# Kernel tuning notes

Hardware: AMD Instinct MI355X
Metric: run time of the kernel (lower is better)

Reference implementation:

```python
import jax, jax.numpy as jnp
import numpy as np

B, T, C = 2, 2048, 1024
H = 16
D = C // H  # head_dim = 64
SCALE = D ** -0.5


def setup_inputs() -> dict:
    key = jax.random.key(0)
    ks = jax.random.split(key, 5)
    s = 0.02
    return {
        "x": jax.random.normal(ks[0], (B, T, C), dtype=jnp.float32),
        "w_qkv": jax.random.normal(ks[1], (C, 3 * C), dtype=jnp.float32) * s,
        "b_qkv": jnp.zeros((3 * C,), dtype=jnp.float32),
        "w_proj": jax.random.normal(ks[2], (C, C), dtype=jnp.float32) * s,
        "b_proj": jnp.zeros((C,), dtype=jnp.float32),
    }


def reference(x, w_qkv, b_qkv, w_proj, b_proj):
    Bx, Tx, Cx = x.shape
    qkv = x @ w_qkv + b_qkv                      # [B,T,3C]
    q, k, v = jnp.split(qkv, 3, axis=-1)
    # [B,T,C] -> [B,H,T,D]
    q = q.reshape(Bx, Tx, H, D).transpose(0, 2, 1, 3)
    k = k.reshape(Bx, Tx, H, D).transpose(0, 2, 1, 3)
    v = v.reshape(Bx, Tx, H, D).transpose(0, 2, 1, 3)
    attn = jnp.einsum('bhqd,bhkd->bhqk', q, k) * SCALE
    causal = jnp.tril(jnp.ones((Tx, Tx), dtype=bool))
    attn = jnp.where(causal[None, None], attn, -jnp.inf)
    attn = jax.nn.softmax(attn, axis=-1)
    out = jnp.einsum('bhqk,bhkd->bhqd', attn, v)  # [B,H,T,D]
    out = out.transpose(0, 2, 1, 3).reshape(Bx, Tx, Cx)
    return out @ w_proj + b_proj
```

## Files before the change

### kernel.cpp

```cpp
#include <hip/hip_runtime.h>
#include <hip/hip_bf16.h>
#include <math.h>

#define T_SEQ 2048
#define NHEAD 16
#define HDIM  64
#define CDIM  1024
#define KDIM  1024
#define SCALE_L2E 0.1803368801111204f

typedef __attribute__((ext_vector_type(8))) short bf16x8;
typedef __attribute__((ext_vector_type(4))) float f32x4;
typedef __attribute__((ext_vector_type(16))) float f32x16;
typedef __attribute__((ext_vector_type(8))) unsigned short u16x8;
typedef __attribute__((ext_vector_type(4))) unsigned int u32x4;

__device__ __forceinline__ unsigned short f2bf(float f) {
    unsigned int u = __builtin_bit_cast(unsigned int, f);
    u += 0x7fffu + ((u >> 16) & 1u);
    return (unsigned short)(u >> 16);
}
__device__ __forceinline__ unsigned int cvt_pk_bf16(float lo, float hi_) {
    unsigned int r;
    asm("v_cvt_pk_bf16_f32 %0, %1, %2" : "=v"(r) : "v"(lo), "v"(hi_));
    return r;
}
__device__ __forceinline__ void pl32swap(unsigned int &a, unsigned int &b) {
    asm("v_permlane32_swap_b32 %0, %1" : "+v"(a), "+v"(b));
}
__device__ __forceinline__ void gld16(const unsigned short* g, unsigned short* l) {
    __builtin_amdgcn_global_load_lds(
        (const __attribute__((address_space(1))) unsigned int*)g,
        (__attribute__((address_space(3))) unsigned int*)l,
        16, 0, 0);
}

__global__ __launch_bounds__(256) void prep_all(
    const float* __restrict__ x,  unsigned short* __restrict__ Xb,
    const float* __restrict__ wq, unsigned short* __restrict__ Wqt,
    const float* __restrict__ wp, unsigned short* __restrict__ Wpt)
{
    __shared__ unsigned short Ls[64][72];
    const int bid = blockIdx.x;
    if (bid < 2048) {
        size_t i = ((size_t)bid * 256 + threadIdx.x) * 8;
        float4 a = *(const float4*)(x + i);
        float4 b = *(const float4*)(x + i + 4);
        u32x4 o;
        o[0] = cvt_pk_bf16(a.x, a.y);
        o[1] = cvt_pk_bf16(a.z, a.w);
        o[2] = cvt_pk_bf16(b.x, b.y);
        o[3] = cvt_pk_bf16(b.z, b.w);
        *(u32x4*)(Xb + i) = o;
        return;
    }
    const float* W; unsigned short* Wt; int NC, n0, k0;
    if (bid < 2048 + 768) {
        int b = bid - 2048;
        W = wq; Wt = Wqt; NC = 3072; n0 = (b % 48) * 64; k0 = (b / 48) * 64;
    } else {
        int b = bid - 2816;
        W = wp; Wt = Wpt; NC = 1024; n0 = (b % 16) * 64; k0 = (b / 16) * 64;
    }
    const int t = threadIdx.x;
    {
        int kr = t >> 2, nc = (t & 3) * 16;
        #pragma unroll
        for (int j = 0; j < 4; j++) {
            float4 v = *(const float4*)(W + (size_t)(k0 + kr) * NC + n0 + nc + j * 4);
            Ls[nc + j*4 + 0][kr] = f2bf(v.x);
            Ls[nc + j*4 + 1][kr] = f2bf(v.y);
            Ls[nc + j*4 + 2][kr] = f2bf(v.z);
            Ls[nc + j*4 + 3][kr] = f2bf(v.w);
        }
    }
    __syncthreads();
    {
        int nr = t >> 2, kc = (t & 3) * 16;
        u16x8 o0 = *(const u16x8*)&Ls[nr][kc];
        u16x8 o1 = *(const u16x8*)&Ls[nr][kc + 8];
        *(u16x8*)(Wt + (size_t)(n0 + nr) * KDIM + k0 + kc)     = o0;
        *(u16x8*)(Wt + (size_t)(n0 + nr) * KDIM + k0 + kc + 8) = o1;
    }
}

template<int NC, int EPI>
__global__ __launch_bounds__(256) void gemm_k(
    const unsigned short* __restrict__ A, const unsigned short* __restrict__ Wt,
    const float* __restrict__ bias, float* __restrict__ Of,
    unsigned short* __restrict__ Qb, unsigned short* __restrict__ Kb,
    unsigned short* __restrict__ Vt)
{
    __shared__ unsigned short As[128 * 64];
    __shared__ unsigned short Bs[128 * 64];

    const int tid  = threadIdx.x;
    const int lane = tid & 63;
    const int wid  = tid >> 6;
    const int m0 = blockIdx.x * 128;
    const int n0 = blockIdx.y * 128;
    const int wm = (wid >> 1) * 64;
    const int wn = (wid & 1) * 64;
    const int rl = lane & 15;

    const int r8 = lane >> 3, s8 = lane & 7;
    const int swzs = (s8 ^ r8) * 8;

    f32x4 acc[4][4] = {};

    for (int k0 = 0; k0 < KDIM; k0 += 64) {
        #pragma unroll
        for (int c = 0; c < 4; c++) {
            int row = (wid << 5) + (c << 3) + r8;
            gld16(A  + (size_t)(m0 + row) * KDIM + k0 + swzs, &As[(size_t)((wid<<5)+(c<<3)) * 64]);
            gld16(Wt + (size_t)(n0 + row) * KDIM + k0 + swzs, &Bs[(size_t)((wid<<5)+(c<<3)) * 64]);
        }
        __syncthreads();
        #pragma unroll
        for (int kc = 0; kc < 2; kc++) {
            const int sb = kc * 4 + (lane >> 4);
            bf16x8 af[4], bfr[4];
            #pragma unroll
            for (int f = 0; f < 4; f++) {
                int sw = (sb ^ (rl & 7)) * 8;
                af[f]  = *(const bf16x8*)&As[(wm + f*16 + rl) * 64 + sw];
                bfr[f] = *(const bf16x8*)&Bs[(wn + f*16 + rl) * 64 + sw];
            }
            __builtin_amdgcn_s_setprio(1);
            #pragma unroll
            for (int i = 0; i < 4; i++)
                #pragma unroll
                for (int j = 0; j < 4; j++)
                    acc[i][j] = __builtin_amdgcn_mfma_f32_16x16x32_bf16(af[i], bfr[j], acc[i][j], 0, 0, 0);
            __builtin_amdgcn_s_setprio(0);
        }
        __syncthreads();
    }

    #pragma unroll
    for (int j = 0; j < 4; j++) {
        int gn = n0 + wn + j*16 + rl;
        float bv = bias[gn];
        #pragma unroll
        for (int i = 0; i < 4; i++) {
            int gm0 = m0 + wm + i*16 + (lane >> 4) * 4;
            #pragma unroll
            for (int r = 0; r < 4; r++) {
                float v = acc[i][j][r] + bv;
                int gm = gm0 + r;
                if (EPI == 0) {
                    int which = gn >> 10;
                    int cw = gn & 1023;
                    int h = cw >> 6, d = cw & 63;
                    int b = gm >> 11, t = gm & 2047;
                    size_t bh = (size_t)(b * NHEAD + h);
                    if (which == 0)      Qb[(bh * T_SEQ + t) * HDIM + d] = f2bf(v * SCALE_L2E);
                    else if (which == 1) Kb[(bh * T_SEQ + t) * HDIM + d] = f2bf(v);
                    else                 Vt[(bh * HDIM + d) * T_SEQ + t] = f2bf(v);
                } else {
                    Of[(size_t)gm * NC + gn] = v;
                }
            }
        }
    }
}

__global__ __launch_bounds__(128, 4) void attn_k(
    const unsigned short* __restrict__ Qb, const unsigned short* __restrict__ Kb,
    const unsigned short* __restrict__ Vt, unsigned short* __restrict__ AO)
{
    __shared__ unsigned short sbuf[2 * 4096];

    const int tid  = threadIdx.x;
    const int lane = tid & 63;
    const int w    = tid >> 6;
    const int bh   = blockIdx.x;
    const int qt   = 63 - blockIdx.y;
    const int ql   = lane & 31;
    const int hi   = lane >> 5;
    const int qg   = (qt << 5) + ql;

    const unsigned short* Qp = Qb + (size_t)bh * T_SEQ * HDIM;
    const unsigned short* Kp = Kb + (size_t)bh * T_SEQ * HDIM;
    const unsigned short* Vp = Vt + (size_t)bh * HDIM * T_SEQ;

    unsigned short* kbuf = sbuf + w * 4096;
    const char* kbB = (const char*)kbuf;
    const char* vbB = (const char*)(kbuf + 2048);

    const int r8 = lane >> 3, s8 = lane & 7;
    const int key = s8 ^ r8;
    const unsigned short* kSrc = Kp + (size_t)r8 * HDIM + (key << 3);
    const unsigned short* vSrc = Vp + (size_t)((key >> 2) * 32 + r8) * T_SEQ + (key & 3) * 8;

    auto issue_tile = [&](int t) {
        #pragma unroll
        for (int c = 0; c < 4; c++)
            gld16(kSrc + ((size_t)t << 11) + (c << 9), kbuf + (c << 9));
        #pragma unroll
        for (int c = 0; c < 4; c++)
            gld16(vSrc + ((size_t)c << 14) + (t << 5), kbuf + 2048 + (c << 9));
    };

    bf16x8 qf[4];
    #pragma unroll
    for (int dc = 0; dc < 4; dc++)
        qf[dc] = *(const bf16x8*)(Qp + (size_t)qg * HDIM + dc*16 + hi*8);

    float l_run = 0.f;
    f32x16 o0 = {}, o1 = {};

    if (w <= qt) {
        issue_tile(w);
        for (int t = w; t <= qt; t += 2) {
            asm volatile("s_waitcnt vmcnt(0)" ::: "memory");
            __builtin_amdgcn_sched_barrier(0);

            bf16x8 kf[4];
            #pragma unroll
            for (int dc = 0; dc < 4; dc++)
                kf[dc] = *(const bf16x8*)(kbB + ql*128 + (((dc << 1 | hi) ^ (ql & 7)) << 4));
            bf16x8 v00 = *(const bf16x8*)(vbB + ql*128 + (((0 + hi) ^ (ql & 7)) << 4));
            bf16x8 v01 = *(const bf16x8*)(vbB + ql*128 + (((2 + hi) ^ (ql & 7)) << 4));
            bf16x8 v10 = *(const bf16x8*)(vbB + ql*128 + (((4 + hi) ^ (ql & 7)) << 4));
            bf16x8 v11 = *(const bf16x8*)(vbB + ql*128 + (((6 + hi) ^ (ql & 7)) << 4));
            asm volatile("s_waitcnt lgkmcnt(0)" ::: "memory");
            __builtin_amdgcn_sched_barrier(0);

            if (t + 2 <= qt) issue_tile(t + 2);

            f32x16 s = {};
            __builtin_amdgcn_s_setprio(1);
            #pragma unroll
            for (int dc = 0; dc < 4; dc++)
                s = __builtin_amdgcn_mfma_f32_32x32x16_bf16(kf[dc], qf[dc], s, 0, 0, 0);
            __builtin_amdgcn_s_setprio(0);

            float p[16];
            if (t == qt) {
                #pragma unroll
                for (int r = 0; r < 16; r++) {
                    int kv = (t << 5) + (r & 3) + 8 * (r >> 2) + 4 * hi;
                    p[r] = (kv > qg) ? 0.f : exp2f(s[r]);
                }
            } else {
                #pragma unroll
                for (int r = 0; r < 16; r++) p[r] = exp2f(s[r]);
            }
            float r0 = (p[0]  + p[1])  + (p[2]  + p[3]);
            float r1 = (p[4]  + p[5])  + (p[6]  + p[7]);
            float r2 = (p[8]  + p[9])  + (p[10] + p[11]);
            float r3 = (p[12] + p[13]) + (p[14] + p[15]);
            l_run += (r0 + r1) + (r2 + r3);

            unsigned int c[8];
            #pragma unroll
            for (int i = 0; i < 8; i++) c[i] = cvt_pk_bf16(p[2*i], p[2*i+1]);
            pl32swap(c[0], c[2]);  pl32swap(c[1], c[3]);
            pl32swap(c[4], c[6]);  pl32swap(c[5], c[7]);
            u32x4 b0 = {c[0], c[1], c[2], c[3]};
            u32x4 b1 = {c[4], c[5], c[6], c[7]};
            bf16x8 pf0 = __builtin_bit_cast(bf16x8, b0);
            bf16x8 pf1 = __builtin_bit_cast(bf16x8, b1);

            __builtin_amdgcn_s_setprio(1);
            o0 = __builtin_amdgcn_mfma_f32_32x32x16_bf16(v00, pf0, o0, 0, 0, 0);
            o0 = __builtin_amdgcn_mfma_f32_32x32x16_bf16(v01, pf1, o0, 0, 0, 0);
            o1 = __builtin_amdgcn_mfma_f32_32x32x16_bf16(v10, pf0, o1, 0, 0, 0);
            o1 = __builtin_amdgcn_mfma_f32_32x32x16_bf16(v11, pf1, o1, 0, 0, 0);
            __builtin_amdgcn_s_setprio(0);
        }
    }

    __syncthreads();
    float* lf = (float*)sbuf;
    if (w == 1) {
        #pragma unroll
        for (int j = 0; j < 4; j++) {
            f32x4 a = { o0[4*j], o0[4*j+1], o0[4*j+2], o0[4*j+3] };
            *(f32x4*)(lf + (size_t)(j*64 + lane) * 4) = a;
        }
        #pragma unroll
        for (int j = 0; j < 4; j++) {
            f32x4 a = { o1[4*j], o1[4*j+1], o1[4*j+2], o1[4*j+3] };
            *(f32x4*)(lf + (size_t)((4+j)*64 + lane) * 4) = a;
        }
        lf[2048 + lane] = l_run;
    }
    __syncthreads();
    if (w == 0) {
        float l_all = l_run + lf[2048 + lane];
        l_all += __shfl_xor(l_all, 32);
        float linv = 1.f / l_all;
        const int b = bh >> 4, h = bh & 15;
        unsigned short* aop = AO + ((size_t)(b * T_SEQ + qg)) * CDIM + h * HDIM;
        #pragma unroll
        for (int qd = 0; qd < 4; qd++) {
            f32x4 x0 = *(const f32x4*)(lf + (size_t)(qd*64 + lane) * 4);
            f32x4 x1 = *(const f32x4*)(lf + (size_t)((4+qd)*64 + lane) * 4);
            uint2 w0, w1;
            w0.x = cvt_pk_bf16((o0[4*qd+0] + x0[0]) * linv, (o0[4*qd+1] + x0[1]) * linv);
            w0.y = cvt_pk_bf16((o0[4*qd+2] + x0[2]) * linv, (o0[4*qd+3] + x0[3]) * linv);
            w1.x = cvt_pk_bf16((o1[4*qd+0] + x1[0]) * linv, (o1[4*qd+1] + x1[1]) * linv);
            w1.y = cvt_pk_bf16((o1[4*qd+2] + x1[2]) * linv, (o1[4*qd+3] + x1[3]) * linv);
            *(uint2*)(aop + qd*8 + hi*4)      = w0;
            *(uint2*)(aop + 32 + qd*8 + hi*4) = w1;
        }
    }
}

extern "C" void kernel_launch(void* const* d_in, const int* in_sizes, int n_in,
                              void* d_out, int out_size, void* d_ws, size_t ws_size,
                              hipStream_t stream) {
    const float* x      = (const float*)d_in[0];
    const float* w_qkv  = (const float*)d_in[1];
    const float* b_qkv  = (const float*)d_in[2];
    const float* w_proj = (const float*)d_in[3];
    const float* b_proj = (const float*)d_in[4];
    float* out = (float*)d_out;

    const size_t MI = (size_t)1 << 20;
    unsigned short* base = (unsigned short*)d_ws;
    unsigned short* Qb  = base;
    unsigned short* Kb  = base + 4*MI;
    unsigned short* Vt  = base + 8*MI;
    unsigned short* Wqt = base + 12*MI;
    unsigned short* Wpt = base + 15*MI;
    unsigned short* Xb  = base + 16*MI;
    unsigned short* AO  = Xb;

    prep_all<<<dim3(3072), 256, 0, stream>>>(x, Xb, w_qkv, Wqt, w_proj, Wpt);
    gemm_k<3072, 0><<<dim3(32, 24), 256, 0, stream>>>(
        Xb, Wqt, b_qkv, nullptr, Qb, Kb, Vt);
    attn_k<<<dim3(32, 64), 128, 0, stream>>>(Qb, Kb, Vt, AO);
    gemm_k<1024, 1><<<dim3(32, 8), 256, 0, stream>>>(
        AO, Wpt, b_proj, out, nullptr, nullptr, nullptr);
}
```

Before: 110.5 us.

## Pair short and long causal query tiles per attention block for load balance

The attention kernel now runs 256 threads per block as two wave pairs. One pair handles query tile by and the other handles tile 63-by, so every block carries roughly the same causal work, and the grid shrinks from 64 to 32 in y. This targets tail imbalance from blocks with uneven work and lowers the block count. The cost is doubled shared memory per block (32 KB plus the l buffer), which may limit occupancy.

```diff
diff --git a/kernel.cpp b/kernel.cpp
--- a/kernel.cpp
+++ b/kernel.cpp
@@ -165,17 +165,21 @@
     }
 }
 
-__global__ __launch_bounds__(128, 4) void attn_k(
+__global__ __launch_bounds__(256, 4) void attn_k(
     const unsigned short* __restrict__ Qb, const unsigned short* __restrict__ Kb,
     const unsigned short* __restrict__ Vt, unsigned short* __restrict__ AO)
 {
-    __shared__ unsigned short sbuf[2 * 4096];
+    __shared__ unsigned short sbuf[4 * 4096];
+    __shared__ float mlbuf[2 * 64];
 
     const int tid  = threadIdx.x;
     const int lane = tid & 63;
     const int w    = tid >> 6;
+    const int pair = w >> 1;
+    const int par  = w & 1;
     const int bh   = blockIdx.x;
-    const int qt   = 63 - blockIdx.y;
+    const int by   = blockIdx.y;
+    const int qt   = pair ? (63 - by) : by;
     const int ql   = lane & 31;
     const int hi   = lane >> 5;
     const int qg   = (qt << 5) + ql;
@@ -210,9 +214,9 @@
     float l_run = 0.f;
     f32x16 o0 = {}, o1 = {};
 
-    if (w <= qt) {
-        issue_tile(w);
-        for (int t = w; t <= qt; t += 2) {
+    if (par <= qt) {
+        issue_tile(par);
+        for (int t = par; t <= qt; t += 2) {
             asm volatile("s_waitcnt vmcnt(0)" ::: "memory");
             __builtin_amdgcn_sched_barrier(0);
 
@@ -273,31 +277,31 @@
     }
 
     __syncthreads();
-    float* lf = (float*)sbuf;
-    if (w == 1) {
+    float* plf = (float*)(sbuf + pair * 8192);
+    if (par == 1) {
         #pragma unroll
         for (int j = 0; j < 4; j++) {
             f32x4 a = { o0[4*j], o0[4*j+1], o0[4*j+2], o0[4*j+3] };
-            *(f32x4*)(lf + (size_t)(j*64 + lane) * 4) = a;
+            *(f32x4*)(plf + (size_t)(j*64 + lane) * 4) = a;
         }
         #pragma unroll
         for (int j = 0; j < 4; j++) {
             f32x4 a = { o1[4*j], o1[4*j+1], o1[4*j+2], o1[4*j+3] };
-            *(f32x4*)(lf + (size_t)((4+j)*64 + lane) * 4) = a;
-        }
-        lf[2048 + lane] = l_run;
+            *(f32x4*)(plf + (size_t)((4+j)*64 + lane) * 4) = a;
+        }
+        mlbuf[pair * 64 + lane] = l_run;
     }
     __syncthreads();
-    if (w == 0) {
-        float l_all = l_run + lf[2048 + lane];
+    if (par == 0) {
+        float l_all = l_run + mlbuf[pair * 64 + lane];
         l_all += __shfl_xor(l_all, 32);
         float linv = 1.f / l_all;
         const int b = bh >> 4, h = bh & 15;
         unsigned short* aop = AO + ((size_t)(b * T_SEQ + qg)) * CDIM + h * HDIM;
         #pragma unroll
         for (int qd = 0; qd < 4; qd++) {
-            f32x4 x0 = *(const f32x4*)(lf + (size_t)(qd*64 + lane) * 4);
-            f32x4 x1 = *(const f32x4*)(lf + (size_t)((4+qd)*64 + lane) * 4);
+            f32x4 x0 = *(const f32x4*)(plf + (size_t)(qd*64 + lane) * 4);
+            f32x4 x1 = *(const f32x4*)(plf + (size_t)((4+qd)*64 + lane) * 4);
             uint2 w0, w1;
             w0.x = cvt_pk_bf16((o0[4*qd+0] + x0[0]) * linv, (o0[4*qd+1] + x0[1]) * linv);
             w0.y = cvt_pk_bf16((o0[4*qd+2] + x0[2]) * linv, (o0[4*qd+3] + x0[3]) * linv);
@@ -332,7 +336,7 @@
     prep_all<<<dim3(3072), 256, 0, stream>>>(x, Xb, w_qkv, Wqt, w_proj, Wpt);
     gemm_k<3072, 0><<<dim3(32, 24), 256, 0, stream>>>(
         Xb, Wqt, b_qkv, nullptr, Qb, Kb, Vt);
-    attn_k<<<dim3(32, 64), 128, 0, stream>>>(Qb, Kb, Vt, AO);
+    attn_k<<<dim3(32, 32), 256, 0, stream>>>(Qb, Kb, Vt, AO);
     gemm_k<1024, 1><<<dim3(32, 8), 256, 0, stream>>>(
         AO, Wpt, b_proj, out, nullptr, nullptr, nullptr);
 }
```

Measured after the change: 110.0 us. About the same (-0.4%).
